# Kernel optimization log

Measured on AMD Instinct MI355X. Metric: run time of the kernel, lower is better.

## Reference

```python
import jax, jax.numpy as jnp
import numpy as np

H = 12          # num heads
D = 768         # hidden size
DH = D // H     # size per head
FF = 3072       # intermediate size
EPS = 1e-11


def gelu(x):
    # tanh approximation, matching the TF source exactly
    c = np.sqrt(2.0 / np.pi).astype(np.float32)
    return x * 0.5 * (1.0 + jnp.tanh(c * (x + 0.044715 * jnp.power(x, 3))))


def layer_norm(x, gamma, beta):
    mean = jnp.mean(x, axis=-1, keepdims=True)
    var = jnp.mean(jnp.square(x - mean), axis=-1, keepdims=True)
    return (x - mean) * jax.lax.rsqrt(var + EPS) * gamma + beta


def setup_inputs() -> dict:
    key = jax.random.key(0)
    ks = jax.random.split(key, 12)
    B, S = 16, 512
    std = 0.02
    inp = {
        "x": jax.random.normal(ks[0], (B, S, D), jnp.float32),
        "mask": jnp.ones((B, S), dtype=bool),
        "Wq": jax.random.normal(ks[1], (D, D), jnp.float32) * std,
        "bq": jnp.zeros((D,), jnp.float32),
        "Wk": jax.random.normal(ks[2], (D, D), jnp.float32) * std,
        "bk": jnp.zeros((D,), jnp.float32),
        "Wv": jax.random.normal(ks[3], (D, D), jnp.float32) * std,
        "bv": jnp.zeros((D,), jnp.float32),
        "Wo": jax.random.normal(ks[4], (D, D), jnp.float32) * std,
        "bo": jnp.zeros((D,), jnp.float32),
        "g1": jnp.ones((D,), jnp.float32),
        "b1": jnp.zeros((D,), jnp.float32),
        "Wi": jax.random.normal(ks[5], (D, FF), jnp.float32) * std,
        "bi": jnp.zeros((FF,), jnp.float32),
        "Wo2": jax.random.normal(ks[6], (FF, D), jnp.float32) * std,
        "bo2": jnp.zeros((D,), jnp.float32),
        "g2": jnp.ones((D,), jnp.float32),
        "b2": jnp.zeros((D,), jnp.float32),
    }
    return inp


def reference(x, mask, Wq, bq, Wk, bk, Wv, bv, Wo, bo, g1, b1, Wi, bi, Wo2, bo2, g2, b2):
    B, S, _ = x.shape
    # QKV projections
    q = (x @ Wq + bq).reshape(B, S, H, DH)
    k = (x @ Wk + bk).reshape(B, S, H, DH)
    v = (x @ Wv + bv).reshape(B, S, H, DH)
    # scaled dot-product attention scores [B, H, S, S]
    scores = jnp.einsum("bqhd,bkhd->bhqk", q, k) / np.sqrt(DH).astype(np.float32)
    # key-side mask, applied as score * m + (1 - m) * -100 (per original source)
    m = mask[:, None, None, :].astype(jnp.float32)
    scores = scores * m + (1.0 - m) * (-100.0)
    probs = jax.nn.softmax(scores, axis=-1)
    attn = jnp.einsum("bhqk,bkhd->bqhd", probs, v).reshape(B, S, D)
    # tf.boolean_mask with all-True mask -> flatten batch and seq dims
    attn = attn.reshape(B * S, D)
    x_flat = x.reshape(B * S, D)
    # attention output projection + residual + LN
    attn_out = layer_norm(attn @ Wo + bo + x_flat, g1, b1)
    # FFN: gelu dense then output dense + residual + LN
    inter = gelu(attn_out @ Wi + bi)
    out = layer_norm(inter @ Wo2 + bo2 + attn_out, g2, b2)
    return out
```

## Files before the change

kernel.cpp:

```cpp
#include <hip/hip_runtime.h>


#define DEV __device__ __forceinline__

typedef unsigned short u16;
typedef unsigned int   u32;
typedef __bf16 bf16x8 __attribute__((ext_vector_type(8)));
typedef float  f32x4  __attribute__((ext_vector_type(4)));
typedef unsigned short u16x8 __attribute__((ext_vector_type(8)));
typedef unsigned short u16x4 __attribute__((ext_vector_type(4)));

DEV u16 f2bf(float f) {
    u32 u = __builtin_bit_cast(u32, f);
    u += 0x7fffu + ((u >> 16) & 1u);
    return (u16)(u >> 16);
}
DEV float bf2f(u16 u) { u32 x = (u32)u << 16; return __builtin_bit_cast(float, x); }

DEV float gelu_f(float x) {
    float u = 0.7978845608028654f * (x + 0.044715f * x * x * x);
    float e = __expf(2.f * u);
    return 0.5f * x * (2.f - 2.f / (e + 1.f));
}

DEV void gload16(const void* gsrc, void* ldst) {
    __builtin_amdgcn_global_load_lds(
        (__attribute__((address_space(1))) void*)(void*)(const_cast<void*>(gsrc)),
        (__attribute__((address_space(3))) void*)ldst, 16, 0, 0);
}

DEV f32x4 MFMA(bf16x8 a, bf16x8 b, f32x4 c) {
    return __builtin_amdgcn_mfma_f32_16x16x32_bf16(a, b, c, 0, 0, 0);
}

__global__ __launch_bounds__(256) void prep(
    const float* __restrict__ x, const float* __restrict__ Wq,
    const float* __restrict__ Wk, const float* __restrict__ Wv,
    const float* __restrict__ Wo, const float* __restrict__ Wi,
    const float* __restrict__ Wo2, const float* __restrict__ bq,
    const float* __restrict__ bk, const float* __restrict__ bv,
    u16* __restrict__ Xb, u16* __restrict__ WqkvT, u16* __restrict__ WoT,
    u16* __restrict__ WiT, u16* __restrict__ Wo2T, float* __restrict__ bqkv) {
    __shared__ float tile[32][33];
    int bid = blockIdx.x, t = threadIdx.x;
    if (bid < 6144) {
        int i = (bid * 256 + t) * 4;
        f32x4 v = *(const f32x4*)(x + i);
        u16x4 o;
        o.x = f2bf(v.x); o.y = f2bf(v.y); o.z = f2bf(v.z); o.w = f2bf(v.w);
        *(u16x4*)(Xb + i) = o;
        return;
    }
    bid -= 6144;
    if (bid >= 6912) {
        int i = (bid - 6912) * 256 + t;
        if (i < 2304)
            bqkv[i] = (i < 768) ? bq[i] : (i < 1536 ? bk[i - 768] : bv[i - 1536]);
        return;
    }
    const float* in; u16* out; int R, C, bx, by;
    if (bid < 1728) {
        int w = bid / 576, idx = bid % 576;
        in = (w == 0) ? Wq : (w == 1) ? Wk : Wv;
        out = WqkvT + (size_t)w * 768 * 768;
        R = 768; C = 768; bx = idx % 24; by = idx / 24;
    } else if (bid < 2304) {
        int idx = bid - 1728;
        in = Wo; out = WoT; R = 768; C = 768; bx = idx % 24; by = idx / 24;
    } else if (bid < 4608) {
        int idx = bid - 2304;
        in = Wi; out = WiT; R = 768; C = 3072; bx = idx % 96; by = idx / 96;
    } else {
        int idx = bid - 4608;
        in = Wo2; out = Wo2T; R = 3072; C = 768; bx = idx % 24; by = idx / 24;
    }
    int tx = t & 31, ty = t >> 5;
    int r0 = by * 32, c0 = bx * 32;
#pragma unroll
    for (int i = 0; i < 4; i++)
        tile[ty + i * 8][tx] = in[(size_t)(r0 + ty + i * 8) * C + c0 + tx];
    __syncthreads();
#pragma unroll
    for (int i = 0; i < 4; i++)
        out[(size_t)(c0 + ty + i * 8) * R + r0 + tx] = f2bf(tile[tx][ty + i * 8]);
}

template <int EPI>
DEV void gemm_c3_body(const u16* __restrict__ A, const u16* __restrict__ BT,
                      const float* __restrict__ bias, void* __restrict__ Cout,
                      int N, int K, int ntn) {
    __shared__ __align__(16) char smem[49152];
    const int t = threadIdx.x, lane = t & 63, wid = t >> 6;
    const int nwg = gridDim.x, bid = blockIdx.x;
    const int swzb = ((nwg & 7) == 0) ? ((bid & 7) * (nwg >> 3) + (bid >> 3)) : bid;
    const int tm = swzb / ntn, tn = swzb % ntn;
    const int wm = wid >> 1, wn = wid & 1;

    f32x4 acc[4][4];
#pragma unroll
    for (int i = 0; i < 4; i++)
#pragma unroll
        for (int j = 0; j < 4; j++) acc[i][j] = f32x4{0.f, 0.f, 0.f, 0.f};

    const int NT = K >> 5;
    const u16* Ab = A + (size_t)tm * 128 * K;
    const u16* Bb = BT + (size_t)tn * 128 * K;

    int sr[2], sc[2];
#pragma unroll
    for (int j = 0; j < 2; j++) {
        int X = t * 16 + j * 4096;
        int Y = X ^ (((X >> 7) & 7) << 4);
        sr[j] = Y >> 6; sc[j] = (Y & 63) >> 1;
    }
    const u16* pA0 = Ab + (size_t)sr[0] * K + sc[0];
    const u16* pA1 = Ab + (size_t)sr[1] * K + sc[1];
    const u16* pB0 = Bb + (size_t)sr[0] * K + sc[0];
    const u16* pB1 = Bb + (size_t)sr[1] * K + sc[1];
    const int d0 = wid * 1024, d1 = wid * 1024 + 4096;

    const int g16 = (lane >> 4) << 4;
    const int rA = wm * 64 + (lane & 15);
    const int rB = wn * 64 + (lane & 15);
    const int aoff = (rA * 64 + g16) ^ (((rA >> 1) & 7) << 4);
    const int boff = 8192 + ((rB * 64 + g16) ^ (((rB >> 1) & 7) << 4));

#define STG(TT)                                                       \
    {                                                                 \
        char* s_ = smem + ((TT) % 3) * 16384;                         \
        int ko_ = (TT) * 32;                                          \
        gload16(pA0 + ko_, s_ + d0);                                  \
        gload16(pA1 + ko_, s_ + d1);                                  \
        gload16(pB0 + ko_, s_ + 8192 + d0);                           \
        gload16(pB1 + ko_, s_ + 8192 + d1);                           \
    }

    STG(0) STG(1)
    asm volatile("s_waitcnt vmcnt(4)" ::: "memory");
    __builtin_amdgcn_s_barrier();
    asm volatile("" ::: "memory");

    for (int tt = 0; tt < NT; ++tt) {
        if (tt + 2 < NT) STG(tt + 2)
        const char* buf = smem + (tt % 3) * 16384;
        bf16x8 af[4], bfr[4];
#pragma unroll
        for (int mi = 0; mi < 4; mi++) af[mi] = *(const bf16x8*)(buf + aoff + mi * 1024);
#pragma unroll
        for (int ni = 0; ni < 4; ni++) bfr[ni] = *(const bf16x8*)(buf + boff + ni * 1024);
        __builtin_amdgcn_s_setprio(1);
#pragma unroll
        for (int mi = 0; mi < 4; mi++)
#pragma unroll
            for (int ni = 0; ni < 4; ni++)
                acc[mi][ni] = MFMA(af[mi], bfr[ni], acc[mi][ni]);
        __builtin_amdgcn_s_setprio(0);
        if (tt + 1 < NT) {
            if (tt + 2 < NT) asm volatile("s_waitcnt vmcnt(4)" ::: "memory");
            else             asm volatile("s_waitcnt vmcnt(0)" ::: "memory");
        }
        __builtin_amdgcn_s_barrier();
        asm volatile("" ::: "memory");
    }
#undef STG

    const int r0 = tm * 128 + wm * 64, c0 = tn * 128 + wn * 64;
    float bcol[4];
#pragma unroll
    for (int ni = 0; ni < 4; ni++) bcol[ni] = bias[c0 + ni * 16 + (lane & 15)];
#pragma unroll
    for (int mi = 0; mi < 4; mi++) {
#pragma unroll
        for (int r = 0; r < 4; r++) {
            int gr = r0 + mi * 16 + ((lane >> 4) << 2) + r;
#pragma unroll
            for (int ni = 0; ni < 4; ni++) {
                int gc = c0 + ni * 16 + (lane & 15);
                float v = acc[mi][ni][r] + bcol[ni];
                if constexpr (EPI == 2) v = gelu_f(v);
                ((u16*)Cout)[(size_t)gr * N + gc] = f2bf(v);
            }
        }
    }
}

__global__ __launch_bounds__(256, 3) void g3_qkv(const u16* A, const u16* BT,
                                                 const float* bias, void* C,
                                                 int N, int K, int ntn) {
    gemm_c3_body<0>(A, BT, bias, C, N, K, ntn);
}
__global__ __launch_bounds__(256, 3) void g3_wo(const u16* A, const u16* BT,
                                                const float* bias, void* C,
                                                int N, int K, int ntn) {
    gemm_c3_body<0>(A, BT, bias, C, N, K, ntn);
}
__global__ __launch_bounds__(256, 3) void g3_ffn1(const u16* A, const u16* BT,
                                                  const float* bias, void* C,
                                                  int N, int K, int ntn) {
    gemm_c3_body<2>(A, BT, bias, C, N, K, ntn);
}
__global__ __launch_bounds__(256, 3) void g3_ffn2(const u16* A, const u16* BT,
                                                  const float* bias, void* C,
                                                  int N, int K, int ntn) {
    gemm_c3_body<0>(A, BT, bias, C, N, K, ntn);
}

__global__ __launch_bounds__(256) void attn_kernel(const u16* __restrict__ QKV,
                                                   u16* __restrict__ attnb) {
    __shared__ __align__(16) char sm[24576];
    char* Ks = sm;
    char* Vt = sm + 8192;
    const int t = threadIdx.x, lane = t & 63, wid = t >> 6;
    const int qt = blockIdx.x, bh = blockIdx.y;
    const int b = bh / 12, h = bh % 12;
    const size_t base = (size_t)b * 512 * 2304;
    char* Pw = sm + 16384 + wid * 2048;

    bf16x8 aq[2];
    {
        int qrow = qt * 64 + wid * 16 + (lane & 15);
        const u16* qp = QKV + base + (size_t)qrow * 2304 + h * 64 + ((lane >> 4) << 3);
        aq[0] = *(const bf16x8*)qp;
        aq[1] = *(const bf16x8*)(qp + 32);
    }
    f32x4 oacc[4];
#pragma unroll
    for (int g = 0; g < 4; g++) oacc[g] = f32x4{0.f, 0.f, 0.f, 0.f};
    float mrun[4] = {-1e30f, -1e30f, -1e30f, -1e30f};
    float lrun[4] = {0.f, 0.f, 0.f, 0.f};

    for (int kt = 0; kt < 8; ++kt) {
        __syncthreads();
#pragma unroll
        for (int i = 0; i < 2; i++) {
            int cw = wid * 2 + i;
            int o = cw * 1024 + lane * 16;
            int row = o >> 7;
            int cb = (o & 127) ^ ((row & 7) << 4);
            gload16(QKV + base + (size_t)(kt * 64 + row) * 2304 + 768 + h * 64 + (cb >> 1),
                    Ks + cw * 1024);
        }
        {
            int key = t & 63, dh0 = wid * 16;
            const u16* vp = QKV + base + (size_t)(kt * 64 + key) * 2304 + 1536 + h * 64 + dh0;
            u16x8 v0 = *(const u16x8*)vp;
            u16x8 v1 = *(const u16x8*)(vp + 8);
#pragma unroll
            for (int j = 0; j < 8; j++) {
                int dh = dh0 + j;
                *(u16*)(Vt + dh * 128 + ((key * 2) ^ ((dh & 7) << 4))) = v0[j];
            }
#pragma unroll
            for (int j = 0; j < 8; j++) {
                int dh = dh0 + 8 + j;
                *(u16*)(Vt + dh * 128 + ((key * 2) ^ ((dh & 7) << 4))) = v1[j];
            }
        }
        __syncthreads();

        f32x4 sacc[4];
#pragma unroll
        for (int ni = 0; ni < 4; ni++) sacc[ni] = f32x4{0.f, 0.f, 0.f, 0.f};
#pragma unroll
        for (int ni = 0; ni < 4; ni++) {
            int row = ni * 16 + (lane & 15);
#pragma unroll
            for (int ks = 0; ks < 2; ks++) {
                int cb = (ks * 64 + ((lane >> 4) << 4)) ^ ((row & 7) << 4);
                bf16x8 bk = *(const bf16x8*)(Ks + row * 128 + cb);
                sacc[ni] = MFMA(aq[ks], bk, sacc[ni]);
            }
        }
#pragma unroll
        for (int ni = 0; ni < 4; ni++)
#pragma unroll
            for (int r = 0; r < 4; r++) sacc[ni][r] *= 0.125f;

#pragma unroll
        for (int r = 0; r < 4; r++) {
            float pm = fmaxf(fmaxf(sacc[0][r], sacc[1][r]), fmaxf(sacc[2][r], sacc[3][r]));
            pm = fmaxf(pm, __shfl_xor(pm, 1));
            pm = fmaxf(pm, __shfl_xor(pm, 2));
            pm = fmaxf(pm, __shfl_xor(pm, 4));
            pm = fmaxf(pm, __shfl_xor(pm, 8));
            float mnew = fmaxf(mrun[r], pm);
            float sf = __expf(mrun[r] - mnew);
            mrun[r] = mnew;
            lrun[r] *= sf;
#pragma unroll
            for (int g = 0; g < 4; g++) oacc[g][r] *= sf;
            int prow = ((lane >> 4) << 2) + r;
            float ps = 0.f;
#pragma unroll
            for (int ni = 0; ni < 4; ni++) {
                float p = __expf(sacc[ni][r] - mnew);
                ps += p;
                int col = ni * 16 + (lane & 15);
                *(u16*)(Pw + prow * 128 + ((col * 2) ^ ((prow & 7) << 4))) = f2bf(p);
            }
            ps += __shfl_xor(ps, 1);
            ps += __shfl_xor(ps, 2);
            ps += __shfl_xor(ps, 4);
            ps += __shfl_xor(ps, 8);
            lrun[r] += ps;
        }
        __syncthreads();

#pragma unroll
        for (int ks = 0; ks < 2; ks++) {
            int prow = lane & 15;
            int pcb = (ks * 64 + ((lane >> 4) << 4)) ^ ((prow & 7) << 4);
            bf16x8 ap = *(const bf16x8*)(Pw + prow * 128 + pcb);
#pragma unroll
            for (int g = 0; g < 4; g++) {
                int vrow = g * 16 + (lane & 15);
                int vcb = (ks * 64 + ((lane >> 4) << 4)) ^ ((vrow & 7) << 4);
                bf16x8 bv = *(const bf16x8*)(Vt + vrow * 128 + vcb);
                oacc[g] = MFMA(ap, bv, oacc[g]);
            }
        }
    }

#pragma unroll
    for (int g = 0; g < 4; g++)
#pragma unroll
        for (int r = 0; r < 4; r++) {
            int qrow = qt * 64 + wid * 16 + ((lane >> 4) << 2) + r;
            float o = oacc[g][r] / lrun[r];
            attnb[(size_t)(b * 512 + qrow) * 768 + h * 64 + g * 16 + (lane & 15)] = f2bf(o);
        }
}

template <int RESBF, int OUTF>
__global__ __launch_bounds__(256) void ln_t(const u16* __restrict__ Yb,
                                            const void* __restrict__ res,
                                            const float* __restrict__ g,
                                            const float* __restrict__ bta,
                                            void* __restrict__ out) {
    int row = blockIdx.x, t = threadIdx.x, lane = t & 63, wid = t >> 6;
    const u16* y = Yb + (size_t)row * 768;
    float v[3];
#pragma unroll
    for (int i = 0; i < 3; i++) {
        int c = t + i * 256;
        float rv = RESBF ? bf2f(((const u16*)res)[(size_t)row * 768 + c])
                         : ((const float*)res)[(size_t)row * 768 + c];
        v[i] = bf2f(y[c]) + rv;
    }

    float s = v[0] + v[1] + v[2];
#pragma unroll
    for (int o = 32; o; o >>= 1) s += __shfl_xor(s, o);
    __shared__ float sm[4];
    __shared__ float bc[2];
    if (lane == 0) sm[wid] = s;
    __syncthreads();
    if (t == 0) bc[0] = (sm[0] + sm[1] + sm[2] + sm[3]) * (1.f / 768.f);
    __syncthreads();
    float mean = bc[0];

    float q = 0.f;
#pragma unroll
    for (int i = 0; i < 3; i++) { float d = v[i] - mean; q += d * d; }
#pragma unroll
    for (int o = 32; o; o >>= 1) q += __shfl_xor(q, o);
    if (lane == 0) sm[wid] = q;
    __syncthreads();
    if (t == 0) bc[1] = rsqrtf((sm[0] + sm[1] + sm[2] + sm[3]) * (1.f / 768.f) + 1e-11f);
    __syncthreads();
    float rs = bc[1];
#pragma unroll
    for (int i = 0; i < 3; i++) {
        int c = t + i * 256;
        float o = (v[i] - mean) * rs * g[c] + bta[c];
        if constexpr (OUTF)
            ((float*)out)[(size_t)row * 768 + c] = o;
        else
            ((u16*)out)[(size_t)row * 768 + c] = f2bf(o);
    }
}

extern "C" void kernel_launch(void* const* d_in, const int* in_sizes, int n_in,
                              void* d_out, int out_size, void* d_ws, size_t ws_size,
                              hipStream_t stream) {
    const float* x   = (const float*)d_in[0];
    const float* Wq  = (const float*)d_in[2];
    const float* bq  = (const float*)d_in[3];
    const float* Wk  = (const float*)d_in[4];
    const float* bk  = (const float*)d_in[5];
    const float* Wv  = (const float*)d_in[6];
    const float* bv  = (const float*)d_in[7];
    const float* Wo  = (const float*)d_in[8];
    const float* bo  = (const float*)d_in[9];
    const float* g1  = (const float*)d_in[10];
    const float* b1  = (const float*)d_in[11];
    const float* Wi  = (const float*)d_in[12];
    const float* bi  = (const float*)d_in[13];
    const float* Wo2 = (const float*)d_in[14];
    const float* bo2 = (const float*)d_in[15];
    const float* g2  = (const float*)d_in[16];
    const float* b2  = (const float*)d_in[17];

    char* w = (char*)d_ws;
    size_t off = 0;
    auto alloc = [&](size_t n) { size_t o = off; off += (n + 255) & ~(size_t)255; return o; };
    size_t oXb    = alloc((size_t)8192 * 768 * 2);
    size_t oWqkvT = alloc((size_t)2304 * 768 * 2);
    size_t oWoT   = alloc((size_t)768 * 768 * 2);
    size_t oWiT   = alloc((size_t)3072 * 768 * 2);
    size_t oWo2T  = alloc((size_t)768 * 3072 * 2);
    size_t oBqkv  = alloc((size_t)2304 * 4);
    size_t oR0    = alloc((size_t)8192 * 3072 * 2);
    size_t oYb    = alloc((size_t)8192 * 768 * 2);
    size_t oAob   = alloc((size_t)8192 * 768 * 2);
    (void)ws_size; (void)in_sizes; (void)n_in; (void)out_size;

    u16*   Xb    = (u16*)(w + oXb);
    u16*   WqkvT = (u16*)(w + oWqkvT);
    u16*   WoT   = (u16*)(w + oWoT);
    u16*   WiT   = (u16*)(w + oWiT);
    u16*   Wo2T  = (u16*)(w + oWo2T);
    float* bqkv  = (float*)(w + oBqkv);
    u16*   QKV   = (u16*)(w + oR0);
    u16*   attnb = (u16*)(w + oR0 + (size_t)8192 * 2304 * 2);
    u16*   inter = (u16*)(w + oR0);
    u16*   Yb    = (u16*)(w + oYb);
    u16*   aob   = (u16*)(w + oAob);

    prep<<<13065, 256, 0, stream>>>(x, Wq, Wk, Wv, Wo, Wi, Wo2, bq, bk, bv,
                                    Xb, WqkvT, WoT, WiT, Wo2T, bqkv);
    g3_qkv<<<1152, 256, 0, stream>>>(Xb, WqkvT, bqkv, QKV, 2304, 768, 18);
    attn_kernel<<<dim3(8, 192), 256, 0, stream>>>(QKV, attnb);
    g3_wo<<<384, 256, 0, stream>>>(attnb, WoT, bo, Yb, 768, 768, 6);
    ln_t<0, 0><<<8192, 256, 0, stream>>>(Yb, x, g1, b1, aob);
    g3_ffn1<<<1536, 256, 0, stream>>>(aob, WiT, bi, inter, 3072, 768, 24);
    g3_ffn2<<<384, 256, 0, stream>>>(inter, Wo2T, bo2, Yb, 768, 3072, 6);
    ln_t<1, 1><<<8192, 256, 0, stream>>>(Yb, aob, g2, b2, (float*)d_out);
}
```

Measured before the change: 257.7 us.

## Use 256x128 tiles with 8 waves and triple-buffered LDS for QKV/FFN1, fuse residual into GEMM

Adds a new GEMM body with 512 threads computing 256x128 output tiles, using a 3-stage LDS ring buffer, for the QKV and FFN1 projections. The larger tile raises operand reuse and halves the block count. The residual add also moves from the layernorm kernels into the Wo and FFN2 GEMM epilogues, so LN reads one bf16 input instead of two. The cost is higher LDS use (72KB) and lower occupancy per CU. The residual sum is now rounded to bf16 before the layernorm, which slightly changes numerics.

```diff
diff --git a/kernel.cpp b/kernel.cpp
--- a/kernel.cpp
+++ b/kernel.cpp
@@ -86,9 +86,117 @@
 }
 
 template <int EPI>
-DEV void gemm_c3_body(const u16* __restrict__ A, const u16* __restrict__ BT,
+DEV void gemm_g4_body(const u16* __restrict__ A, const u16* __restrict__ BT,
                       const float* __restrict__ bias, void* __restrict__ Cout,
                       int N, int K, int ntn) {
+    __shared__ __align__(16) char smem[73728];
+    const int t = threadIdx.x, lane = t & 63, wid = t >> 6;
+    const int nwg = gridDim.x, bid = blockIdx.x;
+    const int swzb = ((nwg & 7) == 0) ? ((bid & 7) * (nwg >> 3) + (bid >> 3)) : bid;
+    const int tm = swzb / ntn, tn = swzb % ntn;
+    const int wm = wid >> 1, wn = wid & 1;
+
+    f32x4 acc[4][4];
+#pragma unroll
+    for (int i = 0; i < 4; i++)
+#pragma unroll
+        for (int j = 0; j < 4; j++) acc[i][j] = f32x4{0.f, 0.f, 0.f, 0.f};
+
+    const int NT = K >> 5;
+    const u16* Ab = A + (size_t)tm * 256 * K;
+    const u16* Bb = BT + (size_t)tn * 128 * K;
+
+    int ra[2], ca[2];
+#pragma unroll
+    for (int j = 0; j < 2; j++) {
+        int X = t * 16 + j * 8192;
+        int Y = X ^ (((X >> 7) & 7) << 4);
+        ra[j] = Y >> 6; ca[j] = (Y & 63) >> 1;
+    }
+    const u16* pA0 = Ab + (size_t)ra[0] * K + ca[0];
+    const u16* pA1 = Ab + (size_t)ra[1] * K + ca[1];
+    const u16* pB0 = Bb + (size_t)ra[0] * K + ca[0];
+    const int dA0 = t * 16, dA1 = t * 16 + 8192, dB = 16384 + t * 16;
+
+    const int g16 = (lane >> 4) << 4;
+    const int rA = wm * 64 + (lane & 15);
+    const int rB = wn * 64 + (lane & 15);
+    const int aoff = (rA * 64 + g16) ^ (((rA >> 1) & 7) << 4);
+    const int boff = 16384 + ((rB * 64 + g16) ^ (((rB >> 1) & 7) << 4));
+
+#define STG4(TT)                                                      \
+    {                                                                 \
+        char* s_ = smem + ((TT) % 3) * 24576;                         \
+        int ko_ = (TT) * 32;                                          \
+        gload16(pA0 + ko_, s_ + dA0);                                 \
+        gload16(pA1 + ko_, s_ + dA1);                                 \
+        gload16(pB0 + ko_, s_ + dB);                                  \
+    }
+
+    STG4(0) STG4(1)
+    asm volatile("s_waitcnt vmcnt(3)" ::: "memory");
+    __builtin_amdgcn_s_barrier();
+    asm volatile("" ::: "memory");
+
+    for (int tt = 0; tt < NT; ++tt) {
+        if (tt + 2 < NT) STG4(tt + 2)
+        const char* buf = smem + (tt % 3) * 24576;
+        bf16x8 af[4], bfr[4];
+#pragma unroll
+        for (int mi = 0; mi < 4; mi++) af[mi] = *(const bf16x8*)(buf + aoff + mi * 1024);
+#pragma unroll
+        for (int ni = 0; ni < 4; ni++) bfr[ni] = *(const bf16x8*)(buf + boff + ni * 1024);
+        __builtin_amdgcn_s_setprio(1);
+#pragma unroll
+        for (int mi = 0; mi < 4; mi++)
+#pragma unroll
+            for (int ni = 0; ni < 4; ni++)
+                acc[mi][ni] = MFMA(af[mi], bfr[ni], acc[mi][ni]);
+        __builtin_amdgcn_s_setprio(0);
+        if (tt + 1 < NT) {
+            if (tt + 2 < NT) asm volatile("s_waitcnt vmcnt(3)" ::: "memory");
+            else             asm volatile("s_waitcnt vmcnt(0)" ::: "memory");
+        }
+        __builtin_amdgcn_s_barrier();
+        asm volatile("" ::: "memory");
+    }
+#undef STG4
+
+    const int r0 = tm * 256 + wm * 64, c0 = tn * 128 + wn * 64;
+    float bcol[4];
+#pragma unroll
+    for (int ni = 0; ni < 4; ni++) bcol[ni] = bias[c0 + ni * 16 + (lane & 15)];
+#pragma unroll
+    for (int mi = 0; mi < 4; mi++) {
+#pragma unroll
+        for (int r = 0; r < 4; r++) {
+            int gr = r0 + mi * 16 + ((lane >> 4) << 2) + r;
+#pragma unroll
+            for (int ni = 0; ni < 4; ni++) {
+                int gc = c0 + ni * 16 + (lane & 15);
+                float v = acc[mi][ni][r] + bcol[ni];
+                if constexpr (EPI == 2) v = gelu_f(v);
+                ((u16*)Cout)[(size_t)gr * N + gc] = f2bf(v);
+            }
+        }
+    }
+}
+
+__global__ __launch_bounds__(512, 2) void g4_qkv(const u16* A, const u16* BT,
+                                                 const float* bias, void* C,
+                                                 int N, int K, int ntn) {
+    gemm_g4_body<0>(A, BT, bias, C, N, K, ntn);
+}
+__global__ __launch_bounds__(512, 2) void g4_ffn1(const u16* A, const u16* BT,
+                                                  const float* bias, void* C,
+                                                  int N, int K, int ntn) {
+    gemm_g4_body<2>(A, BT, bias, C, N, K, ntn);
+}
+
+template <int EPI>
+DEV void gemm_c3_body(const u16* __restrict__ A, const u16* __restrict__ BT,
+                      const float* __restrict__ bias, const void* __restrict__ res,
+                      void* __restrict__ Cout, int N, int K, int ntn) {
     __shared__ __align__(16) char smem[49152];
     const int t = threadIdx.x, lane = t & 63, wid = t >> 6;
     const int nwg = gridDim.x, bid = blockIdx.x;
@@ -177,32 +285,25 @@
             for (int ni = 0; ni < 4; ni++) {
                 int gc = c0 + ni * 16 + (lane & 15);
                 float v = acc[mi][ni][r] + bcol[ni];
-                if constexpr (EPI == 2) v = gelu_f(v);
+                if constexpr (EPI == 3)
+                    v += ((const float*)res)[(size_t)gr * N + gc];
+                if constexpr (EPI == 4)
+                    v += bf2f(((const u16*)res)[(size_t)gr * N + gc]);
                 ((u16*)Cout)[(size_t)gr * N + gc] = f2bf(v);
             }
         }
     }
 }
 
-__global__ __launch_bounds__(256, 3) void g3_qkv(const u16* A, const u16* BT,
-                                                 const float* bias, void* C,
-                                                 int N, int K, int ntn) {
-    gemm_c3_body<0>(A, BT, bias, C, N, K, ntn);
-}
 __global__ __launch_bounds__(256, 3) void g3_wo(const u16* A, const u16* BT,
-                                                const float* bias, void* C,
-                                                int N, int K, int ntn) {
-    gemm_c3_body<0>(A, BT, bias, C, N, K, ntn);
-}
-__global__ __launch_bounds__(256, 3) void g3_ffn1(const u16* A, const u16* BT,
-                                                  const float* bias, void* C,
-                                                  int N, int K, int ntn) {
-    gemm_c3_body<2>(A, BT, bias, C, N, K, ntn);
+                                                const float* bias, const void* res,
+                                                void* C, int N, int K, int ntn) {
+    gemm_c3_body<3>(A, BT, bias, res, C, N, K, ntn);
 }
 __global__ __launch_bounds__(256, 3) void g3_ffn2(const u16* A, const u16* BT,
-                                                  const float* bias, void* C,
-                                                  int N, int K, int ntn) {
-    gemm_c3_body<0>(A, BT, bias, C, N, K, ntn);
+                                                  const float* bias, const void* res,
+                                                  void* C, int N, int K, int ntn) {
+    gemm_c3_body<4>(A, BT, bias, res, C, N, K, ntn);
 }
 
 __global__ __launch_bounds__(256) void attn_kernel(const u16* __restrict__ QKV,
@@ -331,29 +432,23 @@
         }
 }
 
-template <int RESBF, int OUTF>
-__global__ __launch_bounds__(256) void ln_t(const u16* __restrict__ Yb,
-                                            const void* __restrict__ res,
+template <int OUTF>
+__global__ __launch_bounds__(256) void ln_s(const u16* __restrict__ S,
                                             const float* __restrict__ g,
                                             const float* __restrict__ bta,
                                             void* __restrict__ out) {
     int row = blockIdx.x, t = threadIdx.x, lane = t & 63, wid = t >> 6;
-    const u16* y = Yb + (size_t)row * 768;
+    const u16* s = S + (size_t)row * 768;
     float v[3];
 #pragma unroll
-    for (int i = 0; i < 3; i++) {
-        int c = t + i * 256;
-        float rv = RESBF ? bf2f(((const u16*)res)[(size_t)row * 768 + c])
-                         : ((const float*)res)[(size_t)row * 768 + c];
-        v[i] = bf2f(y[c]) + rv;
-    }
-
-    float s = v[0] + v[1] + v[2];
-#pragma unroll
-    for (int o = 32; o; o >>= 1) s += __shfl_xor(s, o);
+    for (int i = 0; i < 3; i++) v[i] = bf2f(s[t + i * 256]);
+
+    float sum = v[0] + v[1] + v[2];
+#pragma unroll
+    for (int o = 32; o; o >>= 1) sum += __shfl_xor(sum, o);
     __shared__ float sm[4];
     __shared__ float bc[2];
-    if (lane == 0) sm[wid] = s;
+    if (lane == 0) sm[wid] = sum;
     __syncthreads();
     if (t == 0) bc[0] = (sm[0] + sm[1] + sm[2] + sm[3]) * (1.f / 768.f);
     __syncthreads();
@@ -429,11 +524,11 @@
 
     prep<<<13065, 256, 0, stream>>>(x, Wq, Wk, Wv, Wo, Wi, Wo2, bq, bk, bv,
                                     Xb, WqkvT, WoT, WiT, Wo2T, bqkv);
-    g3_qkv<<<1152, 256, 0, stream>>>(Xb, WqkvT, bqkv, QKV, 2304, 768, 18);
+    g4_qkv<<<576, 512, 0, stream>>>(Xb, WqkvT, bqkv, QKV, 2304, 768, 18);
     attn_kernel<<<dim3(8, 192), 256, 0, stream>>>(QKV, attnb);
-    g3_wo<<<384, 256, 0, stream>>>(attnb, WoT, bo, Yb, 768, 768, 6);
-    ln_t<0, 0><<<8192, 256, 0, stream>>>(Yb, x, g1, b1, aob);
-    g3_ffn1<<<1536, 256, 0, stream>>>(aob, WiT, bi, inter, 3072, 768, 24);
-    g3_ffn2<<<384, 256, 0, stream>>>(inter, Wo2T, bo2, Yb, 768, 3072, 6);
-    ln_t<1, 1><<<8192, 256, 0, stream>>>(Yb, aob, g2, b2, (float*)d_out);
-}
+    g3_wo<<<384, 256, 0, stream>>>(attnb, WoT, bo, x, Yb, 768, 768, 6);
+    ln_s<0><<<8192, 256, 0, stream>>>(Yb, g1, b1, aob);
+    g4_ffn1<<<768, 512, 0, stream>>>(aob, WiT, bi, inter, 3072, 768, 24);
+    g3_ffn2<<<384, 256, 0, stream>>>(inter, Wo2T, bo2, aob, Yb, 768, 3072, 6);
+    ln_s<1><<<8192, 256, 0, stream>>>(Yb, g2, b2, (float*)d_out);
+}
```

Result: no change. 258.6 us (+0.4%).
